# Kernel optimization log

Measured on AMD Instinct MI355X. Metric: run time of the kernel, lower is better.

The kernel has to match this reference:

```python
import jax, jax.numpy as jnp
import numpy as np

N_NODES = 50000
N_EDGES = 800000
IN_CH, HID_CH, OUT_CH = 256, 128, 64


def setup_inputs() -> dict:
    key = jax.random.key(0)
    k_x, k_e, k_w1, k_w2 = jax.random.split(key, 4)
    x = jax.random.normal(k_x, (N_NODES, IN_CH), dtype=jnp.float32)
    edge_index = jax.random.randint(k_e, (2, N_EDGES), 0, N_NODES, dtype=jnp.int32)
    # Glorot-style init like PyG GCNConv (weight [in, out], bias zeros)
    s1 = float(np.sqrt(6.0 / (IN_CH + HID_CH)))
    s2 = float(np.sqrt(6.0 / (HID_CH + OUT_CH)))
    W1 = jax.random.uniform(k_w1, (IN_CH, HID_CH), jnp.float32, -s1, s1)
    b1 = jnp.zeros((HID_CH,), jnp.float32)
    W2 = jax.random.uniform(k_w2, (HID_CH, OUT_CH), jnp.float32, -s2, s2)
    b2 = jnp.zeros((OUT_CH,), jnp.float32)
    return {"x": x, "edge_index": edge_index, "W1": W1, "b1": b1, "W2": W2, "b2": b2}


def _gcn_conv(x, src, dst, deg_inv_sqrt, W, b, n_nodes):
    """GCNConv with self-loops: D^{-1/2}(A+I)D^{-1/2} X W + b."""
    h = x @ W  # [N, out]
    norm = deg_inv_sqrt[src] * deg_inv_sqrt[dst]          # [E]
    msgs = h[src] * norm[:, None]                          # [E, out] gather
    agg = jax.ops.segment_sum(msgs, dst, num_segments=n_nodes)  # scatter-add
    self_loop = h * (deg_inv_sqrt * deg_inv_sqrt)[:, None]      # self-loop term
    return agg + self_loop + b


def reference(x, edge_index, W1, b1, W2, b2):
    n = x.shape[0]
    src, dst = edge_index[0], edge_index[1]
    # degree includes self-loop (+1), edge weight 1, counted at destination
    deg = jnp.zeros((n,), x.dtype).at[dst].add(1.0) + 1.0
    dis = jax.lax.rsqrt(deg)
    h = jax.nn.relu(_gcn_conv(x, src, dst, dis, W1, b1, n))
    out = jax.nn.relu(_gcn_conv(h, src, dst, dis, W2, b2, n))
    return out
```

## Files before the change

### kernel.cpp

```cpp
#include <hip/hip_runtime.h>

#define N_NODES 50000
#define N_EDGES 800000
#define IN_CH 256
#define HID_CH 128
#define OUT_CH 64
#define CAP 64
#define NBINS 196
#define PCHUNK 3200
#define PBLOCKS 250
#define SWZ_BLOCKS ((IN_CH * HID_CH + HID_CH * OUT_CH) / 256)

typedef _Float16 f16;
typedef _Float16 f16x8 __attribute__((ext_vector_type(8)));
typedef _Float16 f16x2 __attribute__((ext_vector_type(2)));
typedef float f32x4 __attribute__((ext_vector_type(4)));
typedef unsigned short u16;
typedef unsigned int u32;

template <int K, int N>
__device__ __forceinline__ void swz(const float* __restrict__ W, f16* __restrict__ Bsw,
                                    int idx) {
    constexpr int NTILES = N / 16;
    int j = idx & 7;
    int lane = (idx >> 3) & 63;
    int rest = idx >> 9;
    int nt = rest % NTILES;
    int ks = rest / NTILES;
    int k = ks * 32 + (lane >> 4) * 8 + j;
    int n = nt * 16 + (lane & 15);
    Bsw[idx] = (f16)W[(size_t)k * N + n];
}

__global__ __launch_bounds__(256) void k_pre(const int* __restrict__ dst,
                                             int* __restrict__ binCnt, int E,
                                             const float* __restrict__ W1,
                                             const float* __restrict__ W2,
                                             f16* __restrict__ B1,
                                             f16* __restrict__ B2) {
    if ((int)blockIdx.x < PBLOCKS) {
        __shared__ int lcnt[NBINS];
        for (int i = threadIdx.x; i < NBINS; i += 256) lcnt[i] = 0;
        __syncthreads();
        int base = blockIdx.x * PCHUNK;
        int end = min(base + PCHUNK, E);
        for (int i = base + (int)threadIdx.x; i < end; i += 256)
            atomicAdd(&lcnt[dst[i] >> 8], 1);
        __syncthreads();
        for (int i = threadIdx.x; i < NBINS; i += 256)
            if (lcnt[i]) atomicAdd(&binCnt[i], lcnt[i]);
        return;
    }
    int idx = ((int)blockIdx.x - PBLOCKS) * 256 + threadIdx.x;
    if (idx < IN_CH * HID_CH) {
        swz<IN_CH, HID_CH>(W1, B1, idx);
    } else {
        idx -= IN_CH * HID_CH;
        if (idx < HID_CH * OUT_CH) swz<HID_CH, OUT_CH>(W2, B2, idx);
    }
}

__global__ __launch_bounds__(256) void k_scan(const int* __restrict__ binCnt,
                                              int* __restrict__ binStart,
                                              int* __restrict__ binCursor) {
    __shared__ int s[256];
    int t = threadIdx.x;
    int v = t < NBINS ? binCnt[t] : 0;
    s[t] = v;
    __syncthreads();
    for (int ofs = 1; ofs < 256; ofs <<= 1) {
        int add = (t >= ofs) ? s[t - ofs] : 0;
        __syncthreads();
        s[t] += add;
        __syncthreads();
    }
    int excl = s[t] - v;
    if (t < NBINS) { binStart[t] = excl; binCursor[t] = excl; }
    if (t == 0) binStart[NBINS] = N_EDGES;
}

__global__ __launch_bounds__(256) void k_place(const int* __restrict__ src,
                                               const int* __restrict__ dst,
                                               int* __restrict__ binCursor,
                                               u32* __restrict__ ebuf, int E) {
    __shared__ u32 codes[PCHUNK];
    __shared__ int lcnt[NBINS], lbase[NBINS], lcur[NBINS];
    for (int i = threadIdx.x; i < NBINS; i += 256) lcnt[i] = 0;
    __syncthreads();
    int base = blockIdx.x * PCHUNK;
    int m = min(PCHUNK, E - base);
    for (int j = threadIdx.x; j < m; j += 256) {
        u32 d = (u32)dst[base + j];
        codes[j] = (d << 16) | (u32)src[base + j];
        atomicAdd(&lcnt[d >> 8], 1);
    }
    __syncthreads();
    for (int i = threadIdx.x; i < NBINS; i += 256) {
        lbase[i] = atomicAdd(&binCursor[i], lcnt[i]);
        lcur[i] = 0;
    }
    __syncthreads();
    for (int j = threadIdx.x; j < m; j += 256) {
        u32 c = codes[j];
        int b = c >> 24;
        int p = atomicAdd(&lcur[b], 1);
        ebuf[lbase[b] + p] = c;
    }
}

__global__ __launch_bounds__(256) void k_build(const u32* __restrict__ ebuf,
                                               const int* __restrict__ binStart,
                                               int* __restrict__ cnt,
                                               float* __restrict__ dis,
                                               u16* __restrict__ bucket, int N) {
    __shared__ int lcnt[256];
    __shared__ u16 lbuck[256 * CAP];
    int t = threadIdx.x;
    lcnt[t] = 0;
    __syncthreads();
    int b = blockIdx.x;
    int s = binStart[b], e = binStart[b + 1];
    for (int i = s + t; i < e; i += 256) {
        u32 c = ebuf[i];
        int local = (c >> 16) & 255;
        int p = atomicAdd(&lcnt[local], 1);
        if (p < CAP) lbuck[local * CAP + p] = (u16)(c & 0xFFFFu);
    }
    __syncthreads();
    int nodeBase = b << 8;
    if (nodeBase + t < N) {
        cnt[nodeBase + t] = lcnt[t];
        dis[nodeBase + t] = rsqrtf((float)lcnt[t] + 1.0f);
    }
    const uint4* lsrc = (const uint4*)lbuck;
    uint4* gdst = (uint4*)(bucket + (size_t)nodeBase * CAP);
    for (int idx = t; idx < 256 * CAP / 8; idx += 256) {
        int row = idx >> 3;
        if (nodeBase + row < N) gdst[idx] = lsrc[idx];
    }
}

template <int K, int N, bool A_FP32, bool RELU>
__global__ __launch_bounds__(256) void k_gemm(const void* __restrict__ Av,
                                              const f16* __restrict__ Bsw,
                                              const float* __restrict__ dis,
                                              f16* __restrict__ C, int M) {
    constexpr int KSTEPS = K / 32, NTILES = N / 16;
    const int tid = threadIdx.x;
    const int wave = tid >> 6, lane = tid & 63;
    const int quad = lane >> 4, l16 = lane & 15;
    int row = blockIdx.x * 64 + wave * 16 + l16;
    const int rowc = row < M ? row : M - 1;

    f32x4 acc[NTILES];
#pragma unroll
    for (int t = 0; t < NTILES; ++t) acc[t] = (f32x4){0.f, 0.f, 0.f, 0.f};

#pragma unroll
    for (int ks = 0; ks < KSTEPS; ++ks) {
        f16x8 afrag;
        if (A_FP32) {
            const float* A = (const float*)Av;
            const float4* p = (const float4*)(A + (size_t)rowc * K + ks * 32 + quad * 8);
            float4 v0 = p[0], v1 = p[1];
            afrag[0] = (f16)v0.x; afrag[1] = (f16)v0.y;
            afrag[2] = (f16)v0.z; afrag[3] = (f16)v0.w;
            afrag[4] = (f16)v1.x; afrag[5] = (f16)v1.y;
            afrag[6] = (f16)v1.z; afrag[7] = (f16)v1.w;
        } else {
            const f16* A = (const f16*)Av;
            afrag = *(const f16x8*)(A + (size_t)rowc * K + ks * 32 + quad * 8);
            if (RELU) {
#pragma unroll
                for (int j = 0; j < 8; ++j)
                    afrag[j] = afrag[j] > (f16)0 ? afrag[j] : (f16)0;
            }
        }
#pragma unroll
        for (int t = 0; t < NTILES; ++t) {
            f16x8 bfrag = *(const f16x8*)(Bsw + (((size_t)ks * NTILES + t) * 64 + lane) * 8);
            acc[t] = __builtin_amdgcn_mfma_f32_16x16x32_f16(afrag, bfrag, acc[t], 0, 0, 0);
        }
    }

    int rbase = blockIdx.x * 64 + wave * 16 + quad * 4;
#pragma unroll
    for (int r = 0; r < 4; ++r) {
        int gr = rbase + r;
        if (gr < M) {
            float d = dis[gr];
#pragma unroll
            for (int t = 0; t < NTILES; ++t)
                C[(size_t)gr * N + t * 16 + l16] = (f16)(acc[t][r] * d);
        }
    }
}

template <int C, bool RELU_OUT_F32>
__global__ __launch_bounds__(256) void k_pull(const f16* __restrict__ g,
                                              const float* __restrict__ dis,
                                              const float* __restrict__ bias,
                                              const int* __restrict__ cnt,
                                              const u16* __restrict__ bucket,
                                              void* __restrict__ outv, int N) {
    constexpr int LPN = C / 2;
    int tid = blockIdx.x * 256 + threadIdx.x;
    int u = tid / LPN;
    int sub = tid % LPN;
    if (u >= N) return;
    const f16* gp = g + sub * 2;

    f16x2 hv = *(const f16x2*)(gp + (size_t)u * C);
    float a0 = (float)hv[0], a1 = (float)hv[1];

    int n = cnt[u];
    if (n > CAP) n = CAP;
    const u16* row = bucket + u * CAP;

    int k = 0;
    for (; k + 8 <= n; k += 8) {
        uint4 iv = *(const uint4*)(row + k);
        int s0 = iv.x & 0xFFFF, s1 = iv.x >> 16;
        int s2 = iv.y & 0xFFFF, s3 = iv.y >> 16;
        int s4 = iv.z & 0xFFFF, s5 = iv.z >> 16;
        int s6 = iv.w & 0xFFFF, s7 = iv.w >> 16;
        f16x2 v0 = *(const f16x2*)(gp + (size_t)s0 * C);
        f16x2 v1 = *(const f16x2*)(gp + (size_t)s1 * C);
        f16x2 v2 = *(const f16x2*)(gp + (size_t)s2 * C);
        f16x2 v3 = *(const f16x2*)(gp + (size_t)s3 * C);
        f16x2 v4 = *(const f16x2*)(gp + (size_t)s4 * C);
        f16x2 v5 = *(const f16x2*)(gp + (size_t)s5 * C);
        f16x2 v6 = *(const f16x2*)(gp + (size_t)s6 * C);
        f16x2 v7 = *(const f16x2*)(gp + (size_t)s7 * C);
        a0 += ((float)v0[0] + (float)v1[0]) + ((float)v2[0] + (float)v3[0]) +
              (((float)v4[0] + (float)v5[0]) + ((float)v6[0] + (float)v7[0]));
        a1 += ((float)v0[1] + (float)v1[1]) + ((float)v2[1] + (float)v3[1]) +
              (((float)v4[1] + (float)v5[1]) + ((float)v6[1] + (float)v7[1]));
    }
    if (k + 4 <= n) {
        ushort4 s4v = *(const ushort4*)(row + k);
        f16x2 v0 = *(const f16x2*)(gp + (size_t)s4v.x * C);
        f16x2 v1 = *(const f16x2*)(gp + (size_t)s4v.y * C);
        f16x2 v2 = *(const f16x2*)(gp + (size_t)s4v.z * C);
        f16x2 v3 = *(const f16x2*)(gp + (size_t)s4v.w * C);
        a0 += ((float)v0[0] + (float)v1[0]) + ((float)v2[0] + (float)v3[0]);
        a1 += ((float)v0[1] + (float)v1[1]) + ((float)v2[1] + (float)v3[1]);
        k += 4;
    }
    for (; k < n; ++k) {
        f16x2 v = *(const f16x2*)(gp + (size_t)row[k] * C);
        a0 += (float)v[0];
        a1 += (float)v[1];
    }

    float du = dis[u];
    float o0 = fmaf(du, a0, bias[sub * 2]);
    float o1 = fmaf(du, a1, bias[sub * 2 + 1]);
    if (RELU_OUT_F32) {
        float2* out = (float2*)outv;
        out[(size_t)u * LPN + sub] = make_float2(fmaxf(o0, 0.f), fmaxf(o1, 0.f));
    } else {
        f16x2 o;
        o[0] = (f16)o0; o[1] = (f16)o1;
        *(f16x2*)((f16*)outv + (size_t)u * C + sub * 2) = o;
    }
}


extern "C" void kernel_launch(void* const* d_in, const int* in_sizes, int n_in,
                              void* d_out, int out_size, void* d_ws, size_t ws_size,
                              hipStream_t stream) {
    const float* x  = (const float*)d_in[0];
    const int* ei   = (const int*)d_in[1];
    const float* W1 = (const float*)d_in[2];
    const float* b1 = (const float*)d_in[3];
    const float* W2 = (const float*)d_in[4];
    const float* b2 = (const float*)d_in[5];
    float* out = (float*)d_out;

    const int* src = ei;
    const int* dst = ei + N_EDGES;

    char* ws = (char*)d_ws;
    size_t off = 0;
    auto alloc = [&](size_t bytes) -> void* {
        off = (off + 255) & ~(size_t)255;
        void* p = ws + off;
        off += bytes;
        return p;
    };
    int*   binCnt    = (int*)alloc((size_t)NBINS * 4);
    int*   binStart  = (int*)alloc((size_t)(NBINS + 1) * 4);
    int*   binCursor = (int*)alloc((size_t)NBINS * 4);
    u32*   ebuf      = (u32*)alloc((size_t)N_EDGES * 4);
    int*   cnt       = (int*)alloc((size_t)N_NODES * 4);
    float* dis       = (float*)alloc((size_t)N_NODES * 4);
    u16*   bucket    = (u16*)alloc((size_t)N_NODES * CAP * 2);
    f16*   W1sw      = (f16*)alloc((size_t)IN_CH * HID_CH * 2);
    f16*   W2sw      = (f16*)alloc((size_t)HID_CH * OUT_CH * 2);
    f16*   g1        = (f16*)alloc((size_t)N_NODES * HID_CH * 2);
    f16*   agg1      = (f16*)alloc((size_t)N_NODES * HID_CH * 2);
    f16*   g2        = (f16*)alloc((size_t)N_NODES * OUT_CH * 2);

    hipMemsetAsync(binCnt, 0, (size_t)NBINS * 4, stream);

    k_pre<<<PBLOCKS + SWZ_BLOCKS, 256, 0, stream>>>(dst, binCnt, N_EDGES,
                                                    W1, W2, W1sw, W2sw);
    k_scan<<<1, 256, 0, stream>>>(binCnt, binStart, binCursor);
    k_place<<<PBLOCKS, 256, 0, stream>>>(src, dst, binCursor, ebuf, N_EDGES);
    k_build<<<NBINS, 256, 0, stream>>>(ebuf, binStart, cnt, dis, bucket, N_NODES);

    k_gemm<IN_CH, HID_CH, true, false><<<(N_NODES + 63) / 64, 256, 0, stream>>>(
        x, W1sw, dis, g1, N_NODES);
    k_pull<HID_CH, false><<<(N_NODES * (HID_CH / 2) + 255) / 256, 256, 0, stream>>>(
        g1, dis, b1, cnt, bucket, agg1, N_NODES);

    k_gemm<HID_CH, OUT_CH, false, true><<<(N_NODES + 63) / 64, 256, 0, stream>>>(
        agg1, W2sw, dis, g2, N_NODES);
    k_pull<OUT_CH, true><<<(N_NODES * (OUT_CH / 2) + 255) / 256, 256, 0, stream>>>(
        g2, dis, b2, cnt, bucket, out, N_NODES);
}
```

Baseline: 200.8 us.

## Fuse layer-1 aggregation with layer-2 GEMM and fold bin scan into consumers

The separate scan kernel is removed. k_place and k_build each recompute the 196-bin prefix sum locally in shared memory, and binCursor now holds offsets relative to each bin start. The layer-1 pull aggregation (with bias and ReLU) is fused with the layer-2 MFMA GEMM: each 512-thread block aggregates 64 nodes into LDS and multiplies them by W2 directly. This drops the agg1 intermediate round trip through memory and two kernel launches. The cost is redundant scan work in every block and a fused kernel whose gather phase uses 8 waves, with each wave walking 8 nodes serially.

```diff
diff --git a/kernel.cpp b/kernel.cpp
--- a/kernel.cpp
+++ b/kernel.cpp
@@ -17,6 +17,23 @@
 typedef float f32x4 __attribute__((ext_vector_type(4)));
 typedef unsigned short u16;
 typedef unsigned int u32;
+
+__device__ __forceinline__ void local_scan(const int* __restrict__ binCnt,
+                                           int* sc ,
+                                           int* vout ) {
+    int t = threadIdx.x & 255;
+    int v = t < NBINS ? binCnt[t] : 0;
+    sc[t] = v;
+    vout[t] = v;
+    __syncthreads();
+#pragma unroll
+    for (int ofs = 1; ofs < 256; ofs <<= 1) {
+        int add = (t >= ofs) ? sc[t - ofs] : 0;
+        __syncthreads();
+        sc[t] += add;
+        __syncthreads();
+    }
+}
 
 template <int K, int N>
 __device__ __forceinline__ void swz(const float* __restrict__ W, f16* __restrict__ Bsw,
@@ -60,31 +77,15 @@
     }
 }
 
-__global__ __launch_bounds__(256) void k_scan(const int* __restrict__ binCnt,
-                                              int* __restrict__ binStart,
-                                              int* __restrict__ binCursor) {
-    __shared__ int s[256];
-    int t = threadIdx.x;
-    int v = t < NBINS ? binCnt[t] : 0;
-    s[t] = v;
-    __syncthreads();
-    for (int ofs = 1; ofs < 256; ofs <<= 1) {
-        int add = (t >= ofs) ? s[t - ofs] : 0;
-        __syncthreads();
-        s[t] += add;
-        __syncthreads();
-    }
-    int excl = s[t] - v;
-    if (t < NBINS) { binStart[t] = excl; binCursor[t] = excl; }
-    if (t == 0) binStart[NBINS] = N_EDGES;
-}
-
 __global__ __launch_bounds__(256) void k_place(const int* __restrict__ src,
                                                const int* __restrict__ dst,
+                                               const int* __restrict__ binCnt,
                                                int* __restrict__ binCursor,
                                                u32* __restrict__ ebuf, int E) {
     __shared__ u32 codes[PCHUNK];
+    __shared__ int sc[256], vv[256];
     __shared__ int lcnt[NBINS], lbase[NBINS], lcur[NBINS];
+    local_scan(binCnt, sc, vv);
     for (int i = threadIdx.x; i < NBINS; i += 256) lcnt[i] = 0;
     __syncthreads();
     int base = blockIdx.x * PCHUNK;
@@ -96,7 +97,7 @@
     }
     __syncthreads();
     for (int i = threadIdx.x; i < NBINS; i += 256) {
-        lbase[i] = atomicAdd(&binCursor[i], lcnt[i]);
+        lbase[i] = (sc[i] - vv[i]) + atomicAdd(&binCursor[i], lcnt[i]);
         lcur[i] = 0;
     }
     __syncthreads();
@@ -109,17 +110,20 @@
 }
 
 __global__ __launch_bounds__(256) void k_build(const u32* __restrict__ ebuf,
-                                               const int* __restrict__ binStart,
+                                               const int* __restrict__ binCnt,
                                                int* __restrict__ cnt,
                                                float* __restrict__ dis,
                                                u16* __restrict__ bucket, int N) {
+    __shared__ int sc[256], vv[256];
     __shared__ int lcnt[256];
     __shared__ u16 lbuck[256 * CAP];
+    local_scan(binCnt, sc, vv);
     int t = threadIdx.x;
     lcnt[t] = 0;
     __syncthreads();
     int b = blockIdx.x;
-    int s = binStart[b], e = binStart[b + 1];
+    int s = sc[b] - vv[b];
+    int e = sc[b];
     for (int i = s + t; i < e; i += 256) {
         u32 c = ebuf[i];
         int local = (c >> 16) & 255;
@@ -196,21 +200,127 @@
     }
 }
 
-template <int C, bool RELU_OUT_F32>
-__global__ __launch_bounds__(256) void k_pull(const f16* __restrict__ g,
-                                              const float* __restrict__ dis,
-                                              const float* __restrict__ bias,
-                                              const int* __restrict__ cnt,
-                                              const u16* __restrict__ bucket,
-                                              void* __restrict__ outv, int N) {
-    constexpr int LPN = C / 2;
+#define APAD 136
+__global__ __launch_bounds__(512) void k_pullgemm(const f16* __restrict__ g1,
+                                                  const float* __restrict__ dis,
+                                                  const float* __restrict__ b1,
+                                                  const int* __restrict__ cnt,
+                                                  const u16* __restrict__ bucket,
+                                                  const f16* __restrict__ W2sw,
+                                                  f16* __restrict__ g2, int N) {
+    __shared__ f16 As[64][APAD];
+    const int tid = threadIdx.x;
+    const int wave = tid >> 6, lane = tid & 63;
+    const int base = blockIdx.x * 64;
+
+    float bv0 = b1[lane * 2], bv1 = b1[lane * 2 + 1];
+    for (int i = 0; i < 8; ++i) {
+        int uloc = wave * 8 + i;
+        int u = base + uloc;
+        if (u >= N) {
+            f16x2 z; z[0] = (f16)0; z[1] = (f16)0;
+            *(f16x2*)&As[uloc][lane * 2] = z;
+            continue;
+        }
+        const f16* gp = g1 + lane * 2;
+        f16x2 hv = *(const f16x2*)(gp + (size_t)u * HID_CH);
+        float a0 = (float)hv[0], a1 = (float)hv[1];
+
+        int n = cnt[u];
+        if (n > CAP) n = CAP;
+        const u16* row = bucket + u * CAP;
+        int k = 0;
+        for (; k + 8 <= n; k += 8) {
+            uint4 iv = *(const uint4*)(row + k);
+            int s0 = iv.x & 0xFFFF, s1 = iv.x >> 16;
+            int s2 = iv.y & 0xFFFF, s3 = iv.y >> 16;
+            int s4 = iv.z & 0xFFFF, s5 = iv.z >> 16;
+            int s6 = iv.w & 0xFFFF, s7 = iv.w >> 16;
+            f16x2 v0 = *(const f16x2*)(gp + (size_t)s0 * HID_CH);
+            f16x2 v1 = *(const f16x2*)(gp + (size_t)s1 * HID_CH);
+            f16x2 v2 = *(const f16x2*)(gp + (size_t)s2 * HID_CH);
+            f16x2 v3 = *(const f16x2*)(gp + (size_t)s3 * HID_CH);
+            f16x2 v4 = *(const f16x2*)(gp + (size_t)s4 * HID_CH);
+            f16x2 v5 = *(const f16x2*)(gp + (size_t)s5 * HID_CH);
+            f16x2 v6 = *(const f16x2*)(gp + (size_t)s6 * HID_CH);
+            f16x2 v7 = *(const f16x2*)(gp + (size_t)s7 * HID_CH);
+            a0 += ((float)v0[0] + (float)v1[0]) + ((float)v2[0] + (float)v3[0]) +
+                  (((float)v4[0] + (float)v5[0]) + ((float)v6[0] + (float)v7[0]));
+            a1 += ((float)v0[1] + (float)v1[1]) + ((float)v2[1] + (float)v3[1]) +
+                  (((float)v4[1] + (float)v5[1]) + ((float)v6[1] + (float)v7[1]));
+        }
+        if (k + 4 <= n) {
+            ushort4 s4v = *(const ushort4*)(row + k);
+            f16x2 v0 = *(const f16x2*)(gp + (size_t)s4v.x * HID_CH);
+            f16x2 v1 = *(const f16x2*)(gp + (size_t)s4v.y * HID_CH);
+            f16x2 v2 = *(const f16x2*)(gp + (size_t)s4v.z * HID_CH);
+            f16x2 v3 = *(const f16x2*)(gp + (size_t)s4v.w * HID_CH);
+            a0 += ((float)v0[0] + (float)v1[0]) + ((float)v2[0] + (float)v3[0]);
+            a1 += ((float)v0[1] + (float)v1[1]) + ((float)v2[1] + (float)v3[1]);
+            k += 4;
+        }
+        for (; k < n; ++k) {
+            f16x2 v = *(const f16x2*)(gp + (size_t)row[k] * HID_CH);
+            a0 += (float)v[0];
+            a1 += (float)v[1];
+        }
+
+        float du = dis[u];
+        f16x2 o;
+        o[0] = (f16)fmaxf(fmaf(du, a0, bv0), 0.f);
+        o[1] = (f16)fmaxf(fmaf(du, a1, bv1), 0.f);
+        *(f16x2*)&As[uloc][lane * 2] = o;
+    }
+    __syncthreads();
+
+    constexpr int KSTEPS = HID_CH / 32;
+    const int rg = wave >> 1;
+    const int half = wave & 1;
+    const int quad = lane >> 4, l16 = lane & 15;
+
+    f32x4 acc[2];
+    acc[0] = (f32x4){0.f, 0.f, 0.f, 0.f};
+    acc[1] = (f32x4){0.f, 0.f, 0.f, 0.f};
+
+#pragma unroll
+    for (int ks = 0; ks < KSTEPS; ++ks) {
+        f16x8 afrag = *(const f16x8*)&As[rg * 16 + l16][ks * 32 + quad * 8];
+#pragma unroll
+        for (int tt = 0; tt < 2; ++tt) {
+            int nt = half * 2 + tt;
+            f16x8 bfrag = *(const f16x8*)(W2sw + (((size_t)ks * 4 + nt) * 64 + lane) * 8);
+            acc[tt] = __builtin_amdgcn_mfma_f32_16x16x32_f16(afrag, bfrag, acc[tt], 0, 0, 0);
+        }
+    }
+
+    int rbase = base + rg * 16 + quad * 4;
+#pragma unroll
+    for (int r = 0; r < 4; ++r) {
+        int gr = rbase + r;
+        if (gr < N) {
+            float d = dis[gr];
+#pragma unroll
+            for (int tt = 0; tt < 2; ++tt) {
+                int nt = half * 2 + tt;
+                g2[(size_t)gr * OUT_CH + nt * 16 + l16] = (f16)(acc[tt][r] * d);
+            }
+        }
+    }
+}
+
+__global__ __launch_bounds__(256) void k_pull2(const f16* __restrict__ g,
+                                               const float* __restrict__ dis,
+                                               const float* __restrict__ bias,
+                                               const int* __restrict__ cnt,
+                                               const u16* __restrict__ bucket,
+                                               float2* __restrict__ out, int N) {
     int tid = blockIdx.x * 256 + threadIdx.x;
-    int u = tid / LPN;
-    int sub = tid % LPN;
+    int u = tid >> 5;
+    int sub = tid & 31;
     if (u >= N) return;
     const f16* gp = g + sub * 2;
 
-    f16x2 hv = *(const f16x2*)(gp + (size_t)u * C);
+    f16x2 hv = *(const f16x2*)(gp + (size_t)u * OUT_CH);
     float a0 = (float)hv[0], a1 = (float)hv[1];
 
     int n = cnt[u];
@@ -224,14 +334,14 @@
         int s2 = iv.y & 0xFFFF, s3 = iv.y >> 16;
         int s4 = iv.z & 0xFFFF, s5 = iv.z >> 16;
         int s6 = iv.w & 0xFFFF, s7 = iv.w >> 16;
-        f16x2 v0 = *(const f16x2*)(gp + (size_t)s0 * C);
-        f16x2 v1 = *(const f16x2*)(gp + (size_t)s1 * C);
-        f16x2 v2 = *(const f16x2*)(gp + (size_t)s2 * C);
-        f16x2 v3 = *(const f16x2*)(gp + (size_t)s3 * C);
-        f16x2 v4 = *(const f16x2*)(gp + (size_t)s4 * C);
-        f16x2 v5 = *(const f16x2*)(gp + (size_t)s5 * C);
-        f16x2 v6 = *(const f16x2*)(gp + (size_t)s6 * C);
-        f16x2 v7 = *(const f16x2*)(gp + (size_t)s7 * C);
+        f16x2 v0 = *(const f16x2*)(gp + (size_t)s0 * OUT_CH);
+        f16x2 v1 = *(const f16x2*)(gp + (size_t)s1 * OUT_CH);
+        f16x2 v2 = *(const f16x2*)(gp + (size_t)s2 * OUT_CH);
+        f16x2 v3 = *(const f16x2*)(gp + (size_t)s3 * OUT_CH);
+        f16x2 v4 = *(const f16x2*)(gp + (size_t)s4 * OUT_CH);
+        f16x2 v5 = *(const f16x2*)(gp + (size_t)s5 * OUT_CH);
+        f16x2 v6 = *(const f16x2*)(gp + (size_t)s6 * OUT_CH);
+        f16x2 v7 = *(const f16x2*)(gp + (size_t)s7 * OUT_CH);
         a0 += ((float)v0[0] + (float)v1[0]) + ((float)v2[0] + (float)v3[0]) +
               (((float)v4[0] + (float)v5[0]) + ((float)v6[0] + (float)v7[0]));
         a1 += ((float)v0[1] + (float)v1[1]) + ((float)v2[1] + (float)v3[1]) +
@@ -239,16 +349,16 @@
     }
     if (k + 4 <= n) {
         ushort4 s4v = *(const ushort4*)(row + k);
-        f16x2 v0 = *(const f16x2*)(gp + (size_t)s4v.x * C);
-        f16x2 v1 = *(const f16x2*)(gp + (size_t)s4v.y * C);
-        f16x2 v2 = *(const f16x2*)(gp + (size_t)s4v.z * C);
-        f16x2 v3 = *(const f16x2*)(gp + (size_t)s4v.w * C);
+        f16x2 v0 = *(const f16x2*)(gp + (size_t)s4v.x * OUT_CH);
+        f16x2 v1 = *(const f16x2*)(gp + (size_t)s4v.y * OUT_CH);
+        f16x2 v2 = *(const f16x2*)(gp + (size_t)s4v.z * OUT_CH);
+        f16x2 v3 = *(const f16x2*)(gp + (size_t)s4v.w * OUT_CH);
         a0 += ((float)v0[0] + (float)v1[0]) + ((float)v2[0] + (float)v3[0]);
         a1 += ((float)v0[1] + (float)v1[1]) + ((float)v2[1] + (float)v3[1]);
         k += 4;
     }
     for (; k < n; ++k) {
-        f16x2 v = *(const f16x2*)(gp + (size_t)row[k] * C);
+        f16x2 v = *(const f16x2*)(gp + (size_t)row[k] * OUT_CH);
         a0 += (float)v[0];
         a1 += (float)v[1];
     }
@@ -256,14 +366,7 @@
     float du = dis[u];
     float o0 = fmaf(du, a0, bias[sub * 2]);
     float o1 = fmaf(du, a1, bias[sub * 2 + 1]);
-    if (RELU_OUT_F32) {
-        float2* out = (float2*)outv;
-        out[(size_t)u * LPN + sub] = make_float2(fmaxf(o0, 0.f), fmaxf(o1, 0.f));
-    } else {
-        f16x2 o;
-        o[0] = (f16)o0; o[1] = (f16)o1;
-        *(f16x2*)((f16*)outv + (size_t)u * C + sub * 2) = o;
-    }
+    out[(size_t)u * 32 + sub] = make_float2(fmaxf(o0, 0.f), fmaxf(o1, 0.f));
 }
 
 
@@ -289,9 +392,8 @@
         off += bytes;
         return p;
     };
-    int*   binCnt    = (int*)alloc((size_t)NBINS * 4);
-    int*   binStart  = (int*)alloc((size_t)(NBINS + 1) * 4);
-    int*   binCursor = (int*)alloc((size_t)NBINS * 4);
+    int*   binCnt    = (int*)alloc((size_t)NBINS * 2 * 4);
+    int*   binCursor = binCnt + NBINS;
     u32*   ebuf      = (u32*)alloc((size_t)N_EDGES * 4);
     int*   cnt       = (int*)alloc((size_t)N_NODES * 4);
     float* dis       = (float*)alloc((size_t)N_NODES * 4);
@@ -299,24 +401,21 @@
     f16*   W1sw      = (f16*)alloc((size_t)IN_CH * HID_CH * 2);
     f16*   W2sw      = (f16*)alloc((size_t)HID_CH * OUT_CH * 2);
     f16*   g1        = (f16*)alloc((size_t)N_NODES * HID_CH * 2);
-    f16*   agg1      = (f16*)alloc((size_t)N_NODES * HID_CH * 2);
     f16*   g2        = (f16*)alloc((size_t)N_NODES * OUT_CH * 2);
 
-    hipMemsetAsync(binCnt, 0, (size_t)NBINS * 4, stream);
+    hipMemsetAsync(binCnt, 0, (size_t)NBINS * 2 * 4, stream);
 
     k_pre<<<PBLOCKS + SWZ_BLOCKS, 256, 0, stream>>>(dst, binCnt, N_EDGES,
                                                     W1, W2, W1sw, W2sw);
-    k_scan<<<1, 256, 0, stream>>>(binCnt, binStart, binCursor);
-    k_place<<<PBLOCKS, 256, 0, stream>>>(src, dst, binCursor, ebuf, N_EDGES);
-    k_build<<<NBINS, 256, 0, stream>>>(ebuf, binStart, cnt, dis, bucket, N_NODES);
+    k_place<<<PBLOCKS, 256, 0, stream>>>(src, dst, binCnt, binCursor, ebuf, N_EDGES);
+    k_build<<<NBINS, 256, 0, stream>>>(ebuf, binCnt, cnt, dis, bucket, N_NODES);
 
     k_gemm<IN_CH, HID_CH, true, false><<<(N_NODES + 63) / 64, 256, 0, stream>>>(
         x, W1sw, dis, g1, N_NODES);
-    k_pull<HID_CH, false><<<(N_NODES * (HID_CH / 2) + 255) / 256, 256, 0, stream>>>(
-        g1, dis, b1, cnt, bucket, agg1, N_NODES);
-
-    k_gemm<HID_CH, OUT_CH, false, true><<<(N_NODES + 63) / 64, 256, 0, stream>>>(
-        agg1, W2sw, dis, g2, N_NODES);
-    k_pull<OUT_CH, true><<<(N_NODES * (OUT_CH / 2) + 255) / 256, 256, 0, stream>>>(
-        g2, dis, b2, cnt, bucket, out, N_NODES);
-}
+
+    k_pullgemm<<<(N_NODES + 63) / 64, 512, 0, stream>>>(g1, dis, b1, cnt, bucket,
+                                                        W2sw, g2, N_NODES);
+
+    k_pull2<<<(N_NODES * 32 + 255) / 256, 256, 0, stream>>>(g2, dis, b2, cnt, bucket,
+                                                            (float2*)out, N_NODES);
+}
```

Result: no change. 203.3 us (+1.2%).
